# Kernel optimization log

Measured on AMD Instinct MI355X. Metric: run time of the kernel, lower is better.

The kernel has to match this reference:

```python
import jax, jax.numpy as jnp
import numpy as np

B, T, D, H = 4, 2048, 1024, 16
HD = D // H  # head_dim = 64


def setup_inputs() -> dict:
    key = jax.random.key(0)
    k1, k2, k3 = jax.random.split(key, 3)
    x = jax.random.normal(k1, (B, T, D), dtype=jnp.float32)
    # rotary cache: (T, head_dim/2, 2) holding (cos, sin)
    inv_freq = 1.0 / (10000.0 ** (jnp.arange(0, HD, 2, dtype=jnp.float32) / HD))  # (HD/2,)
    t = jnp.arange(T, dtype=jnp.float32)
    freqs = jnp.einsum('t,f->tf', t, inv_freq)  # (T, HD/2)
    rope = jnp.stack([jnp.cos(freqs), jnp.sin(freqs)], axis=-1)  # (T, HD/2, 2)
    # causal boolean attn mask, broadcastable (1,1,T,T)
    mask = jnp.tril(jnp.ones((T, T), dtype=bool))[None, None]
    # params (bias-free linears), scaled like nn.Linear default init
    W_attn = jax.random.normal(k2, (3 * D, D), dtype=jnp.float32) / np.sqrt(D)
    W_proj = jax.random.normal(k3, (D, D), dtype=jnp.float32) / np.sqrt(D)
    return {"x": x, "rope": rope, "mask": mask, "W_attn": W_attn, "W_proj": W_proj}


def apply_rope(x, rope):
    # x: (B, T, H, HD); rope: (T, HD/2, 2)
    b, t, h, hd = x.shape
    xr = x.reshape(b, t, h, hd // 2, 2)
    x1, x2 = xr[..., 0], xr[..., 1]
    cos = rope[None, :, None, :, 0]  # (1, T, 1, HD/2)
    sin = rope[None, :, None, :, 1]
    out = jnp.stack([x1 * cos - x2 * sin, x1 * sin + x2 * cos], axis=-1)
    return out.reshape(b, t, h, hd)


def reference(x, rope, mask, W_attn, W_proj):
    b, t, d = x.shape
    qkv = jnp.einsum('btd,ed->bte', x, W_attn)  # (B, T, 3D)
    q, k, v = jnp.split(qkv, 3, axis=2)
    q = apply_rope(q.reshape(b, t, H, HD), rope)
    k = apply_rope(k.reshape(b, t, H, HD), rope)
    v = v.reshape(b, t, H, HD)
    # (B, H, T, HD)
    q = q.transpose(0, 2, 1, 3)
    k = k.transpose(0, 2, 1, 3)
    v = v.transpose(0, 2, 1, 3)
    scale = 1.0 / np.sqrt(HD)
    scores = jnp.einsum('bhqd,bhkd->bhqk', q, k) * scale
    scores = jnp.where(mask, scores, jnp.finfo(scores.dtype).min)
    attn = jax.nn.softmax(scores, axis=-1)
    o = jnp.einsum('bhqk,bhkd->bhqd', attn, v)
    o = o.transpose(0, 2, 1, 3).reshape(b, t, d)
    return jnp.einsum('btd,ed->bte', o, W_proj)
```

## Files before the change

### kernel.cpp

```cpp
#include <hip/hip_runtime.h>

typedef unsigned short u16;
typedef unsigned int u32;
typedef unsigned long long u64;
typedef __bf16 v8bf __attribute__((ext_vector_type(8)));
typedef __bf16 v4bf __attribute__((ext_vector_type(4)));
typedef float v4f __attribute__((ext_vector_type(4)));
typedef float v16f __attribute__((ext_vector_type(16)));
typedef u32 v4u __attribute__((ext_vector_type(4)));

#define BB 4
#define TT 2048
#define HH 16
#define DD 1024

__device__ __forceinline__ u16 f2bf(float f){
  u32 u = __float_as_uint(f);
  u32 r = u + 0x7FFFu + ((u >> 16) & 1u);
  return (u16)(r >> 16);
}
__device__ __forceinline__ float bf2f(u16 h){ return __uint_as_float(((u32)h) << 16); }
__device__ __forceinline__ v16f z16(){
  v16f z;
#pragma unroll
  for (int i = 0; i < 16; i++) z[i] = 0.f;
  return z;
}
__device__ __forceinline__ u32 cvtpk(float lo, float hi){
  u32 d;
  asm("v_cvt_pk_bf16_f32 %0, %1, %2" : "=v"(d) : "v"(lo), "v"(hi));
  return d;
}
__device__ __forceinline__ void swap32(u32 &a, u32 &b){
  asm volatile("v_permlane32_swap_b32 %0, %1" : "+v"(a), "+v"(b));
}

typedef __attribute__((address_space(1))) const void gas_t;
typedef __attribute__((address_space(3))) void las_t;
__device__ __forceinline__ void gl_lds16(const void* g, void* l){
  __builtin_amdgcn_global_load_lds((gas_t*)g, (las_t*)l, 16, 0, 0);
}

__global__ __launch_bounds__(256) void k_convert(
    const float* __restrict__ x, const float* __restrict__ wa,
    const float* __restrict__ wp, u16* __restrict__ xb,
    u16* __restrict__ wab, u16* __restrict__ wpb){
  int i = blockIdx.x * 256 + threadIdx.x;
  const int nxq = (BB*TT*DD) / 4;
  const int naq = (3*DD*DD) / 4;
  const float* src; u16* dst; int j;
  if (i < nxq)            { src = x;  dst = xb;  j = i; }
  else if (i < nxq + naq) { src = wa; dst = wab; j = i - nxq; }
  else                    { src = wp; dst = wpb; j = i - nxq - naq; }
  float4 v = reinterpret_cast<const float4*>(src)[j];
  u64 p = (u64)f2bf(v.x) | ((u64)f2bf(v.y) << 16)
        | ((u64)f2bf(v.z) << 32) | ((u64)f2bf(v.w) << 48);
  reinterpret_cast<u64*>(dst)[j] = p;
}

__global__ __launch_bounds__(256) void k_gemm_bt(
    const u16* __restrict__ A, const u16* __restrict__ Bt,
    int M, int N, int K, int mode, float* __restrict__ Cf,
    u16* __restrict__ qo, u16* __restrict__ ko, u16* __restrict__ vo){
  __shared__ char smem[32768];
  char* As = smem;
  char* Bs = smem + 16384;
  const int t = threadIdx.x;
  const int lane = t & 63, w = t >> 6;
  const int c = lane & 15, g = lane >> 4;
  const int nbn = N >> 7;
  const int bm = blockIdx.x / nbn, bn = blockIdx.x % nbn;
  const long arow0 = (long)bm * 128;
  const long brow0 = (long)bn * 128;
  const int wrow = (w >> 1) * 64, wcol = (w & 1) * 64;

  v4f acc[4][4];
#pragma unroll
  for (int i = 0; i < 4; i++)
#pragma unroll
    for (int j = 0; j < 4; j++){ v4f z = {0.f,0.f,0.f,0.f}; acc[i][j] = z; }

  for (int k0 = 0; k0 < K; k0 += 64){
    __syncthreads();
#pragma unroll
    for (int i = 0; i < 4; i++){
      int slot = t + i * 256;
      int row  = slot >> 3;
      int cb   = (slot & 7) << 4;
      int scb  = cb ^ ((row & 7) << 4);
      gl_lds16((const char*)A  + ((arow0 + row) * (long)K + k0) * 2 + scb,
               As + ((t & 192) + i * 256) * 16);
      gl_lds16((const char*)Bt + ((brow0 + row) * (long)K + k0) * 2 + scb,
               Bs + ((t & 192) + i * 256) * 16);
    }
    __syncthreads();

    v8bf af[4][2], bfr[4][2];
#pragma unroll
    for (int mt = 0; mt < 4; mt++){
      int row = wrow + mt * 16 + c;
      int sw  = (row & 7) << 4;
#pragma unroll
      for (int ks = 0; ks < 2; ks++)
        af[mt][ks] = *(const v8bf*)(As + row * 128 + ((ks * 64 + g * 16) ^ sw));
    }
#pragma unroll
    for (int nt = 0; nt < 4; nt++){
      int row = wcol + nt * 16 + c;
      int sw  = (row & 7) << 4;
#pragma unroll
      for (int ks = 0; ks < 2; ks++)
        bfr[nt][ks] = *(const v8bf*)(Bs + row * 128 + ((ks * 64 + g * 16) ^ sw));
    }
#pragma unroll
    for (int mt = 0; mt < 4; mt++)
#pragma unroll
      for (int nt = 0; nt < 4; nt++)
#pragma unroll
        for (int ks = 0; ks < 2; ks++)
          acc[mt][nt] = __builtin_amdgcn_mfma_f32_16x16x32_bf16(
              af[mt][ks], bfr[nt][ks], acc[mt][nt], 0, 0, 0);
  }

  if (mode == 1){
#pragma unroll
    for (int mt = 0; mt < 4; mt++)
#pragma unroll
      for (int nt = 0; nt < 4; nt++)
#pragma unroll
        for (int r = 0; r < 4; r++){
          long row = arow0 + wrow + mt * 16 + g * 4 + r;
          long col = brow0 + wcol + nt * 16 + c;
          Cf[row * N + col] = acc[mt][nt][r];
        }
  } else {
    long bb = arow0 >> 11;
#pragma unroll
    for (int mt = 0; mt < 4; mt++)
#pragma unroll
      for (int nt = 0; nt < 4; nt++){
        int e    = (int)brow0 + wcol + nt * 16 + c;
        int tsel = e >> 10;
        int h    = (e >> 6) & 15;
        int d    = e & 63;
        long tpos = (arow0 & 2047) + wrow + mt * 16 + g * 4;
        if (tsel == 2){
          v4bf pk;
#pragma unroll
          for (int r = 0; r < 4; r++) pk[r] = (__bf16)acc[mt][nt][r];
          *(v4bf*)(vo + (((bb * HH + h) * 64 + d) << 11) + tpos) = pk;
        } else {
          u16* dst = tsel ? ko : qo;
#pragma unroll
          for (int r = 0; r < 4; r++)
            dst[((bb * HH + h) * TT + tpos + r) * 64 + d] = f2bf(acc[mt][nt][r]);
        }
      }
  }
}

__global__ __launch_bounds__(256) void k_rope2(
    u16* __restrict__ qb, u16* __restrict__ kb, const float* __restrict__ rope){
  int tid   = blockIdx.x * 256 + threadIdx.x;
  int which = tid >> 20;
  int r     = tid & 1048575;
  int s     = r & 7;
  int row   = r >> 3;
  int tpos  = row & 2047;
  u16* base = (which ? kb : qb) + (long)row * 64 + s * 8;
  int4 w0 = *(const int4*)base;
  float4 r01 = *(const float4*)(rope + tpos * 64 + s * 8);
  float4 r23 = *(const float4*)(rope + tpos * 64 + s * 8 + 4);
  float cs[4] = {r01.x, r01.z, r23.x, r23.z};
  float sn[4] = {r01.y, r01.w, r23.y, r23.w};
  float scale = which ? 1.0f : 0.18033688011112042f;
  int wv[4] = {w0.x, w0.y, w0.z, w0.w};
  int ov[4];
#pragma unroll
  for (int j = 0; j < 4; j++){
    float x1 = bf2f((u16)((u32)wv[j] & 0xffffu));
    float x2 = bf2f((u16)((u32)wv[j] >> 16));
    float oe = (x1 * cs[j] - x2 * sn[j]) * scale;
    float od = (x1 * sn[j] + x2 * cs[j]) * scale;
    ov[j] = (int)((u32)f2bf(oe) | ((u32)f2bf(od) << 16));
  }
  int4 out = {ov[0], ov[1], ov[2], ov[3]};
  *(int4*)base = out;
}

__global__ __launch_bounds__(256) void k_attn(
    const u16* __restrict__ Q, const u16* __restrict__ K,
    const u16* __restrict__ Vt, u16* __restrict__ O){
  __shared__ char smem[16384];
  char* ksm = smem;
  char* vsm = smem + 8192;
  int bx = blockIdx.x;
  int bh = bx & 63;
  int pr = bx >> 6;
  int b = bh >> 4, h = bh & 15;
  const u16* Qb = Q  + (size_t)bh * TT * 64;
  const u16* Kb = K  + (size_t)bh * TT * 64;
  const u16* Vb = Vt + (size_t)bh * 64 * TT;
  const int t = threadIdx.x, lane = t & 63, w = t >> 6;
  const int c = lane & 31, hi = lane >> 5;
  const int swz = (c & 7) << 4;

  for (int pass = 0; pass < 2; pass++){
    int bt = pass ? pr : (15 - pr);
    int q0 = bt * 128;
    int wq0 = q0 + w * 32;

    v8bf qf[4];
    {
      const u16* qrow = Qb + (size_t)(wq0 + c) * 64 + hi * 8;
#pragma unroll
      for (int kc = 0; kc < 4; kc++) qf[kc] = *(const v8bf*)(qrow + kc * 16);
    }

    float m_ = -1e30f, l_ = 0.f;
    v16f accO0 = z16(), accO1 = z16();

    for (int kv0 = 0; kv0 < q0 + 128; kv0 += 64){
      __syncthreads();
#pragma unroll
      for (int i = 0; i < 2; i++){
        int s   = t + i * 256;
        int row = s >> 3;
        int cb  = (s & 7) << 4;
        int scb = cb ^ ((row & 7) << 4);
        gl_lds16((const char*)Kb + (size_t)(kv0 + row) * 128 + scb,
                 ksm + ((t & 192) + i * 256) * 16);
        gl_lds16((const char*)Vb + (size_t)row * (TT * 2) + (size_t)kv0 * 2 + scb,
                 vsm + ((t & 192) + i * 256) * 16);
      }
      __syncthreads();

      if (kv0 <= wq0 + 31){
        v16f s0 = z16(), s1 = z16();
#pragma unroll
        for (int kc = 0; kc < 4; kc++){
          int off = (kc * 32 + hi * 16) ^ swz;
          v8bf a0 = *(const v8bf*)(ksm + c * 128 + off);
          v8bf a1 = *(const v8bf*)(ksm + (32 + c) * 128 + off);
          s0 = __builtin_amdgcn_mfma_f32_32x32x16_bf16(a0, qf[kc], s0, 0, 0, 0);
          s1 = __builtin_amdgcn_mfma_f32_32x32x16_bf16(a1, qf[kc], s1, 0, 0, 0);
        }
        if (kv0 + 63 > wq0){
          int q = wq0 + c;
#pragma unroll
          for (int r = 0; r < 16; r++){
            int crow = (r & 3) + 8 * (r >> 2) + 4 * hi;
            if (kv0 + crow > q)      s0[r] = -1e30f;
            if (kv0 + 32 + crow > q) s1[r] = -1e30f;
          }
        }
        float mx = -1e30f;
#pragma unroll
        for (int r = 0; r < 16; r++){ mx = fmaxf(mx, s0[r]); mx = fmaxf(mx, s1[r]); }
        mx = fmaxf(mx, __shfl_xor(mx, 32, 64));
        if (!__all(mx <= m_)){
          float mn = fmaxf(m_, mx);
          float alpha = __builtin_amdgcn_exp2f(m_ - mn);
          m_ = mn;
          l_ *= alpha;
#pragma unroll
          for (int r = 0; r < 16; r++){ accO0[r] *= alpha; accO1[r] *= alpha; }
        }
        float sum = 0.f;
#pragma unroll
        for (int r = 0; r < 16; r++){
          float p0 = __builtin_amdgcn_exp2f(s0[r] - m_);
          float p1 = __builtin_amdgcn_exp2f(s1[r] - m_);
          s0[r] = p0; s1[r] = p1;
          sum += p0 + p1;
        }
        sum += __shfl_xor(sum, 32, 64);
        l_ += sum;
        v8bf pbf[4];
        {
          u32 wd[16];
#pragma unroll
          for (int i = 0; i < 8; i++) wd[i]     = cvtpk(s0[2*i], s0[2*i+1]);
#pragma unroll
          for (int i = 0; i < 8; i++) wd[8 + i] = cvtpk(s1[2*i], s1[2*i+1]);
          swap32(wd[0], wd[2]);  swap32(wd[1], wd[3]);
          swap32(wd[4], wd[6]);  swap32(wd[5], wd[7]);
          swap32(wd[8], wd[10]); swap32(wd[9], wd[11]);
          swap32(wd[12], wd[14]); swap32(wd[13], wd[15]);
          v4u u0 = {wd[0], wd[1], wd[2], wd[3]};
          v4u u1 = {wd[4], wd[5], wd[6], wd[7]};
          v4u u2 = {wd[8], wd[9], wd[10], wd[11]};
          v4u u3 = {wd[12], wd[13], wd[14], wd[15]};
          pbf[0] = __builtin_bit_cast(v8bf, u0);
          pbf[1] = __builtin_bit_cast(v8bf, u1);
          pbf[2] = __builtin_bit_cast(v8bf, u2);
          pbf[3] = __builtin_bit_cast(v8bf, u3);
        }
#pragma unroll
        for (int kc = 0; kc < 4; kc++){
          int off = (kc * 32 + hi * 16) ^ swz;
          v8bf va0 = *(const v8bf*)(vsm + c * 128 + off);
          v8bf va1 = *(const v8bf*)(vsm + (32 + c) * 128 + off);
          accO0 = __builtin_amdgcn_mfma_f32_32x32x16_bf16(va0, pbf[kc], accO0, 0, 0, 0);
          accO1 = __builtin_amdgcn_mfma_f32_32x32x16_bf16(va1, pbf[kc], accO1, 0, 0, 0);
        }
      }
    }

    float inv = __builtin_amdgcn_rcpf(l_);
    int q = wq0 + c;
    u16* orow = O + ((size_t)(b * TT + q)) * DD + h * 64;
#pragma unroll
    for (int q4 = 0; q4 < 4; q4++){
      v4bf o0, o1;
#pragma unroll
      for (int j = 0; j < 4; j++){
        o0[j] = (__bf16)(accO0[q4 * 4 + j] * inv);
        o1[j] = (__bf16)(accO1[q4 * 4 + j] * inv);
      }
      *(v4bf*)(orow + q4 * 8 + hi * 4)      = o0;
      *(v4bf*)(orow + 32 + q4 * 8 + hi * 4) = o1;
    }
  }
}

extern "C" void kernel_launch(void* const* d_in, const int* in_sizes, int n_in,
                              void* d_out, int out_size, void* d_ws, size_t ws_size,
                              hipStream_t stream){
  const float* x    = (const float*)d_in[0];
  const float* rope = (const float*)d_in[1];
  const float* Wa   = (const float*)d_in[3];
  const float* Wp   = (const float*)d_in[4];

  char* ws = (char*)d_ws;
  u16* xb  = (u16*)(ws);
  u16* wab = (u16*)(ws + (16u << 20));
  u16* wpb = (u16*)(ws + (22u << 20));
  u16* qb  = (u16*)(ws + (24u << 20));
  u16* kb  = (u16*)(ws + (40u << 20));
  u16* vtb = (u16*)(ws + (56u << 20));
  u16* ob  = xb;

  k_convert<<<dim3(12288), dim3(256), 0, stream>>>(x, Wa, Wp, xb, wab, wpb);
  k_gemm_bt<<<dim3(24 * 64), dim3(256), 0, stream>>>(
      xb, wab, 8192, 3072, 1024, 0, nullptr, qb, kb, vtb);
  k_rope2<<<dim3(8192), dim3(256), 0, stream>>>(qb, kb, rope);
  k_attn<<<dim3(512), dim3(256), 0, stream>>>(qb, kb, vtb, ob);
  k_gemm_bt<<<dim3(8 * 64), dim3(256), 0, stream>>>(
      ob, wpb, 8192, 1024, 1024, 1, (float*)d_out, nullptr, nullptr, nullptr);
}
```

Before: 181.4 us.

## Double-buffer K/V tiles in LDS and raise wave priority around MFMA blocks

Shared memory grows to two K and two V buffers. The next 64-row K/V tile is issued into the alternate buffer before computing on the current one, which removes one barrier per iteration and overlaps global-to-LDS loads with the QK and PV MFMAs. The MFMA sections are also wrapped in s_setprio so waves in the matrix phase get issue priority. The cost is double the LDS per block, which may lower occupancy. If the compiler inserts conservative vmcnt waits before the LDS reads, the intended overlap could be lost.

```diff
diff --git a/kernel.cpp b/kernel.cpp
--- a/kernel.cpp
+++ b/kernel.cpp
@@ -191,9 +191,7 @@
 __global__ __launch_bounds__(256) void k_attn(
     const u16* __restrict__ Q, const u16* __restrict__ K,
     const u16* __restrict__ Vt, u16* __restrict__ O){
-  __shared__ char smem[16384];
-  char* ksm = smem;
-  char* vsm = smem + 8192;
+  __shared__ char smem[32768];
   int bx = blockIdx.x;
   int bh = bx & 63;
   int pr = bx >> 6;
@@ -220,23 +218,45 @@
     float m_ = -1e30f, l_ = 0.f;
     v16f accO0 = z16(), accO1 = z16();
 
-    for (int kv0 = 0; kv0 < q0 + 128; kv0 += 64){
+    const int nt = (q0 >> 6) + 2;
+    int cur = 0;
+
+    if (pass) __syncthreads();
+#pragma unroll
+    for (int i = 0; i < 2; i++){
+      int s   = t + i * 256;
+      int row = s >> 3;
+      int scb = ((s & 7) << 4) ^ ((row & 7) << 4);
+      gl_lds16((const char*)Kb + (size_t)row * 128 + scb,
+               smem + ((t & 192) + i * 256) * 16);
+      gl_lds16((const char*)Vb + (size_t)row * (TT * 2) + scb,
+               smem + 16384 + ((t & 192) + i * 256) * 16);
+    }
+
+    for (int it = 0; it < nt; it++){
+      int kv0 = it * 64;
       __syncthreads();
-#pragma unroll
-      for (int i = 0; i < 2; i++){
-        int s   = t + i * 256;
-        int row = s >> 3;
-        int cb  = (s & 7) << 4;
-        int scb = cb ^ ((row & 7) << 4);
-        gl_lds16((const char*)Kb + (size_t)(kv0 + row) * 128 + scb,
-                 ksm + ((t & 192) + i * 256) * 16);
-        gl_lds16((const char*)Vb + (size_t)row * (TT * 2) + (size_t)kv0 * 2 + scb,
-                 vsm + ((t & 192) + i * 256) * 16);
+      if (it + 1 < nt){
+        int nkv = kv0 + 64;
+        char* kd = smem + (cur ^ 1) * 8192;
+        char* vd = smem + 16384 + (cur ^ 1) * 8192;
+#pragma unroll
+        for (int i = 0; i < 2; i++){
+          int s   = t + i * 256;
+          int row = s >> 3;
+          int scb = ((s & 7) << 4) ^ ((row & 7) << 4);
+          gl_lds16((const char*)Kb + (size_t)(nkv + row) * 128 + scb,
+                   kd + ((t & 192) + i * 256) * 16);
+          gl_lds16((const char*)Vb + (size_t)row * (TT * 2) + (size_t)nkv * 2 + scb,
+                   vd + ((t & 192) + i * 256) * 16);
+        }
       }
-      __syncthreads();
 
       if (kv0 <= wq0 + 31){
+        char* ksm = smem + cur * 8192;
+        char* vsm = smem + 16384 + cur * 8192;
         v16f s0 = z16(), s1 = z16();
+        __builtin_amdgcn_s_setprio(1);
 #pragma unroll
         for (int kc = 0; kc < 4; kc++){
           int off = (kc * 32 + hi * 16) ^ swz;
@@ -245,6 +265,7 @@
           s0 = __builtin_amdgcn_mfma_f32_32x32x16_bf16(a0, qf[kc], s0, 0, 0, 0);
           s1 = __builtin_amdgcn_mfma_f32_32x32x16_bf16(a1, qf[kc], s1, 0, 0, 0);
         }
+        __builtin_amdgcn_s_setprio(0);
         if (kv0 + 63 > wq0){
           int q = wq0 + c;
 #pragma unroll
@@ -296,6 +317,7 @@
           pbf[2] = __builtin_bit_cast(v8bf, u2);
           pbf[3] = __builtin_bit_cast(v8bf, u3);
         }
+        __builtin_amdgcn_s_setprio(1);
 #pragma unroll
         for (int kc = 0; kc < 4; kc++){
           int off = (kc * 32 + hi * 16) ^ swz;
@@ -304,7 +326,9 @@
           accO0 = __builtin_amdgcn_mfma_f32_32x32x16_bf16(va0, pbf[kc], accO0, 0, 0, 0);
           accO1 = __builtin_amdgcn_mfma_f32_32x32x16_bf16(va1, pbf[kc], accO1, 0, 0, 0);
         }
+        __builtin_amdgcn_s_setprio(0);
       }
+      cur ^= 1;
     }
 
     float inv = __builtin_amdgcn_rcpf(l_);
```

Result: no change. 183.7 us (+1.2%).
